# Optimization experiments

Hardware: AMD Instinct MI355X
Metric: run time of the kernel (lower is better)

The kernel has to match this reference:

```python
import jax, jax.numpy as jnp
import numpy as np
from jax import lax

B = 1024
T = 32           # length_sec = 384 // (2*2*3*1)
HGT = 7          # height_image = 28 // (1*2*2*1)
CC = 32          # last conv channels
AD = HGT * CC    # abstract_dim = 224
HID = 256        # attention decoder hidden
VOCAB = 29
OUT_LEN = 25


def setup_inputs() -> dict:
    ks = jax.random.split(jax.random.key(0), 24)
    n = lambda k, s, sc=1.0: jax.random.normal(k, s, jnp.float32) * sc
    return {
        "x": n(ks[0], (B, 1, 384, 28)),
        "conv1_w": n(ks[1], (4, 1, 3, 3), 0.2),   "conv1_b": n(ks[2], (4,), 0.1),
        "conv2_w": n(ks[3], (16, 4, 3, 3), 0.2),  "conv2_b": n(ks[4], (16,), 0.1),
        "conv3_w": n(ks[5], (16, 16, 3, 3), 0.2), "conv3_b": n(ks[6], (16,), 0.1),
        "conv4_w": n(ks[7], (32, 16, 3, 3), 0.2), "conv4_b": n(ks[8], (32,), 0.1),
        "h0": n(ks[9], (1, AD)), "c0": n(ks[10], (1, AD)),
        "lstm_Wih": n(ks[11], (4 * AD, AD), 0.05), "lstm_Whh": n(ks[12], (4 * AD, AD), 0.05),
        "lstm_bih": n(ks[13], (4 * AD,), 0.05),    "lstm_bhh": n(ks[14], (4 * AD,), 0.05),
        "att_w": n(ks[15], (1, HID + AD), 0.05),   "att_b": n(ks[16], (1,), 0.05),
        "dec_Wih": n(ks[17], (4 * HID, AD), 0.05), "dec_Whh": n(ks[18], (4 * HID, HID), 0.05),
        "dec_bih": n(ks[19], (4 * HID,), 0.05),    "dec_bhh": n(ks[20], (4 * HID,), 0.05),
        "out_w": n(ks[21], (VOCAB, HID), 0.05),    "out_b": n(ks[22], (VOCAB,), 0.05),
    }


def _lstm_cell(h, c, xt, Wih, Whh, bih, bhh):
    # PyTorch gate order: i, f, g, o
    g = xt @ Wih.T + bih + h @ Whh.T + bhh
    i, f, gg, o = jnp.split(g, 4, axis=-1)
    c = jax.nn.sigmoid(f) * c + jax.nn.sigmoid(i) * jnp.tanh(gg)
    h = jax.nn.sigmoid(o) * jnp.tanh(c)
    return h, c


def reference(x, conv1_w, conv1_b, conv2_w, conv2_b, conv3_w, conv3_b, conv4_w, conv4_b,
              h0, c0, lstm_Wih, lstm_Whh, lstm_bih, lstm_bhh,
              att_w, att_b, dec_Wih, dec_Whh, dec_bih, dec_bhh, out_w, out_b):
    def crp(z, w, b, pool):
        y = lax.conv_general_dilated(z, w, (1, 1), [(1, 1), (1, 1)],
                                     dimension_numbers=('NCHW', 'OIHW', 'NCHW'))
        y = jax.nn.relu(y + b[None, :, None, None])
        win = (1, 1) + pool
        return lax.reduce_window(y, -jnp.inf, lax.max, win, win, 'VALID')

    y1 = crp(x, conv1_w, conv1_b, (2, 1))
    y2 = crp(y1, conv2_w, conv2_b, (2, 2))
    y3 = crp(y2, conv3_w, conv3_b, (3, 2))
    y4 = crp(y3, conv4_w, conv4_b, (1, 1))          # [B, 32, 32, 7]
    Bsz = x.shape[0]
    # y5[b,t,i] = y4[b, i%32, t, i//32]  ==  transpose + reshape (replaces python loop)
    y5 = jnp.transpose(y4, (0, 2, 3, 1)).reshape(Bsz, T, AD)   # [B, T, 224]

    # encoder LSTM (seq-major scan, like torch LSTM)
    def estep(carry, xt):
        h, c = carry
        h, c = _lstm_cell(h, c, xt, lstm_Wih, lstm_Whh, lstm_bih, lstm_bhh)
        return (h, c), h
    h0b = jnp.tile(h0, (Bsz, 1))
    c0b = jnp.tile(c0, (Bsz, 1))
    _, hs = lax.scan(estep, (h0b, c0b), jnp.transpose(y5, (1, 0, 2)))
    y8 = jnp.transpose(hs, (1, 0, 2))                # [B, T, 224]

    # attention decoder: additive score softmax(linear(concat(h, enc)))
    w_h = att_w[0, :HID]     # hidden part
    w_e = att_w[0, HID:]     # encoder part
    enc_score = y8 @ w_e     # [B, T], precomputed once

    def dstep(carry, _):
        h, c = carry
        scores = enc_score + (h @ w_h)[:, None] + att_b[0]      # [B, T]
        alpha = jax.nn.softmax(scores, axis=1)
        ctx = jnp.einsum('bt,btd->bd', alpha, y8)               # [B, 224]
        h, c = _lstm_cell(h, c, ctx, dec_Wih, dec_Whh, dec_bih, dec_bhh)
        return (h, c), h @ out_w.T + out_b                      # [B, 29]

    hdec = jnp.zeros((Bsz, HID), x.dtype)
    _, outs = lax.scan(dstep, (hdec, hdec), None, length=OUT_LEN)  # [25, B, 29]
    return jnp.transpose(outs, (1, 2, 0))            # [B, 29, 25]
```

## Files before the change

kernel.cpp:

```cpp
#include <hip/hip_runtime.h>

typedef unsigned short u16;
typedef unsigned int u32;
typedef unsigned long long u64;
typedef __bf16 bfrag __attribute__((ext_vector_type(8)));
typedef float v4f __attribute__((ext_vector_type(4)));

#define DI __device__ __forceinline__

DI float bf2f(u16 b){ union{u32 u; float f;} c; c.u = ((u32)b)<<16; return c.f; }
DI u16 f2bf(float f){ union{float f; u32 u;} c; c.f=f; u32 u=c.u; return (u16)((u + 0x7FFFu + ((u>>16)&1u))>>16); }
DI float sigm(float x){ return 1.0f/(1.0f+__expf(-x)); }
DI float tanhf_(float x){ float a=fabsf(x); float e=__expf(2.0f*a); float r=1.0f-2.0f/(e+1.0f); return x<0.0f? -r : r; }

__global__ __launch_bounds__(256) void k_cvt2(const float* __restrict__ src, u16* __restrict__ hi,
                                              u16* __restrict__ lo, u32 n){
  u32 i = blockIdx.x*256u + threadIdx.x;
  if (i < n){ float v = src[i]; u16 h = f2bf(v); hi[i] = h; lo[i] = f2bf(v - bf2f(h)); }
}

__global__ __launch_bounds__(256) void k_conv1(const float* __restrict__ x, const float* __restrict__ w,
                                               const float* __restrict__ bias, float* __restrict__ y1q, u32 bbase){
  u32 gid = blockIdx.x*256u + threadIdx.x;
  u32 bl = gid/768u, r = gid - bl*768u;
  u32 oy = r>>2, xg = r&3u;
  const float* xb = x + (u64)(bbase+bl)*10752u;
  float win[4][9];
  #pragma unroll
  for (int rr=0; rr<4; rr++){
    int iy = 2*(int)oy - 1 + rr;
    bool vy = (u32)iy < 384u;
    #pragma unroll
    for (int cc=0; cc<9; cc++){
      int ix = (int)(xg*7u) + cc - 1;
      win[rr][cc] = (vy && (u32)ix < 28u) ? xb[iy*28 + ix] : 0.0f;
    }
  }
  #pragma unroll
  for (int co=0; co<4; co++){
    float wf[9];
    #pragma unroll
    for (int j=0;j<9;j++) wf[j] = w[co*9+j];
    float bc = bias[co];
    float* outp = y1q + ((u64)(bl*4u+co)*192u + oy)*28u + xg*7u;
    #pragma unroll
    for (int ox=0; ox<7; ox++){
      float m = 0.0f;
      #pragma unroll
      for (int py=0; py<2; py++){
        float s = bc;
        #pragma unroll
        for (int dy=0; dy<3; dy++)
          #pragma unroll
          for (int dx=0; dx<3; dx++)
            s += win[py+dy][ox+dx]*wf[dy*3+dx];
        m = fmaxf(m, s);
      }
      outp[ox] = m;
    }
  }
}

__global__ __launch_bounds__(256) void k_conv2(const float* __restrict__ y1q, const float* __restrict__ w,
                                               const float* __restrict__ bias, float* __restrict__ y2q){
  u32 gid = blockIdx.x*256u + threadIdx.x;
  u32 bl = gid/1536u, r = gid - bl*1536u;
  u32 oy = r>>4, xg = (r>>3)&1u, cp = r&7u;
  const float* inb = y1q + (u64)bl*21504u;
  float acc[2][7][4];
  #pragma unroll
  for (int c2=0;c2<2;c2++)
    #pragma unroll
    for (int i=0;i<7;i++){ acc[c2][i][0]=0.f;acc[c2][i][1]=0.f;acc[c2][i][2]=0.f;acc[c2][i][3]=0.f; }
  for (int ci=0; ci<4; ci++){
    float win[4][16];
    const float* pl = inb + ci*5376;
    #pragma unroll
    for (int rr=0; rr<4; rr++){
      int iy = 2*(int)oy - 1 + rr;
      bool vy = (u32)iy < 192u;
      #pragma unroll
      for (int cc=0; cc<16; cc++){
        int ix = (int)(xg*14u) + cc - 1;
        win[rr][cc] = (vy && (u32)ix<28u) ? pl[iy*28+ix] : 0.0f;
      }
    }
    float wf[2][9];
    #pragma unroll
    for (int c2=0;c2<2;c2++)
      #pragma unroll
      for (int j=0;j<9;j++) wf[c2][j] = w[((cp*2u+(u32)c2)*4u+(u32)ci)*9u+j];
    #pragma unroll
    for (int c2=0;c2<2;c2++)
      #pragma unroll
      for (int ol=0; ol<7; ol++)
        #pragma unroll
        for (int py=0; py<2; py++)
          #pragma unroll
          for (int px=0; px<2; px++){
            float s = acc[c2][ol][py*2+px];
            #pragma unroll
            for (int dy=0; dy<3; dy++)
              #pragma unroll
              for (int dx=0; dx<3; dx++)
                s += win[py+dy][2*ol+px+dx]*wf[c2][dy*3+dx];
            acc[c2][ol][py*2+px] = s;
          }
  }
  #pragma unroll
  for (int c2=0;c2<2;c2++){
    u32 co = cp*2u+(u32)c2;
    float bc = bias[co];
    float* outp = y2q + ((u64)(bl*16u+co)*96u + oy)*14u + xg*7u;
    #pragma unroll
    for (int ol=0; ol<7; ol++){
      float m = fmaxf(fmaxf(acc[c2][ol][0],acc[c2][ol][1]), fmaxf(acc[c2][ol][2],acc[c2][ol][3])) + bc;
      outp[ol] = fmaxf(m, 0.0f);
    }
  }
}

__global__ __launch_bounds__(256) void k_conv3(const float* __restrict__ y2q, const float* __restrict__ w,
                                               const float* __restrict__ bias, float* __restrict__ y3, u32 bbase){
  u32 gid = blockIdx.x*256u + threadIdx.x;
  u32 bl = gid/512u, r = gid - bl*512u;
  u32 oy = r>>4, co = r&15u;
  const float* inb = y2q + (u64)bl*21504u;
  float acc[7][6];
  #pragma unroll
  for (int i=0;i<7;i++){
    #pragma unroll
    for (int j=0;j<6;j++) acc[i][j]=0.0f;
  }
  for (int ci=0; ci<16; ci++){
    float win[5][16];
    const float* pl = inb + ci*1344;
    #pragma unroll
    for (int rr=0; rr<5; rr++){
      int iy = 3*(int)oy - 1 + rr;
      bool vy = (u32)iy < 96u;
      #pragma unroll
      for (int cc=0; cc<16; cc++){
        int ix = cc-1;
        win[rr][cc] = (vy && (u32)ix<14u) ? pl[iy*14+ix] : 0.0f;
      }
    }
    float wf[9];
    #pragma unroll
    for (int j=0;j<9;j++) wf[j] = w[((u32)co*16u+(u32)ci)*9u+j];
    #pragma unroll
    for (int ox=0; ox<7; ox++){
      #pragma unroll
      for (int py=0; py<3; py++)
        #pragma unroll
        for (int px=0; px<2; px++){
          float s = acc[ox][py*2+px];
          #pragma unroll
          for (int dy=0; dy<3; dy++)
            #pragma unroll
            for (int dx=0; dx<3; dx++)
              s += win[py+dy][2*ox+px+dx]*wf[dy*3+dx];
          acc[ox][py*2+px] = s;
        }
    }
  }
  float bc = bias[co];
  float* outp = y3 + ((u64)((bbase+bl)*16u+co)*32u + oy)*7u;
  #pragma unroll
  for (int ox=0; ox<7; ox++){
    float m = acc[ox][0];
    #pragma unroll
    for (int j=1;j<6;j++) m = fmaxf(m, acc[ox][j]);
    outp[ox] = fmaxf(m + bc, 0.0f);
  }
}

__global__ __launch_bounds__(256) void k_conv4(const float* __restrict__ y3, const float* __restrict__ w,
                                               const float* __restrict__ bias, float* __restrict__ y5){
  u32 gid = blockIdx.x*256u + threadIdx.x;
  u32 b = gid/512u, r = gid - b*512u;
  u32 oy = r>>4, cp = r&15u;
  u32 co0 = cp*2u;
  const float* inb = y3 + (u64)b*3584u;
  float acc[2][7];
  #pragma unroll
  for (int i=0;i<2;i++){
    #pragma unroll
    for (int j=0;j<7;j++) acc[i][j]=0.0f;
  }
  for (int ci=0; ci<16; ci++){
    float win[3][9];
    const float* pl = inb + ci*224;
    #pragma unroll
    for (int rr=0; rr<3; rr++){
      int iy = (int)oy - 1 + rr;
      bool vy = (u32)iy < 32u;
      #pragma unroll
      for (int cc=0; cc<9; cc++){
        int ix = cc-1;
        win[rr][cc] = (vy && (u32)ix<7u) ? pl[iy*7+ix] : 0.0f;
      }
    }
    #pragma unroll
    for (int c2=0; c2<2; c2++){
      float wf[9];
      #pragma unroll
      for (int j=0;j<9;j++) wf[j] = w[((co0+(u32)c2)*16u+(u32)ci)*9u+j];
      #pragma unroll
      for (int ox=0; ox<7; ox++){
        float s = acc[c2][ox];
        #pragma unroll
        for (int dy=0; dy<3; dy++)
          #pragma unroll
          for (int dx=0; dx<3; dx++)
            s += win[dy][ox+dx]*wf[dy*3+dx];
        acc[c2][ox] = s;
      }
    }
  }
  #pragma unroll
  for (int c2=0; c2<2; c2++){
    float bc = bias[co0+(u32)c2];
    #pragma unroll
    for (int ox=0; ox<7; ox++)
      y5[((u64)b*32u + oy)*224u + (u32)ox*32u + (co0+(u32)c2)] = fmaxf(acc[c2][ox] + bc, 0.0f);
  }
}

__global__ __launch_bounds__(1024) void k_zero(u32* __restrict__ p){
  p[threadIdx.x] = 0u;
}

__global__ __launch_bounds__(512, 4) void k_enc7(const u16* __restrict__ WihHi, const u16* __restrict__ WihLo,
                                                 const u16* __restrict__ WhhHi, const u16* __restrict__ WhhLo,
                                                 const float* __restrict__ bih, const float* __restrict__ bhh,
                                                 const float* __restrict__ y5, const float* __restrict__ h0,
                                                 const float* __restrict__ c0, float* __restrict__ y8,
                                                 u32* __restrict__ eflags){
  __shared__ __align__(16) u16 Ahi[16*456], Alo[16*456];
  __shared__ __align__(16) float gsh[16*132];
  __shared__ __align__(16) float bsh[128];
  u32 tid = threadIdx.x, w = tid>>6, lane = tid&63u, nl = lane&15u, quad = lane>>4;
  u32 bid = blockIdx.x, g = bid & 63u, q = bid >> 6;
  u32 b0 = g*16u, hc0 = q*32u;
  if (tid < 128u){
    u32 gi = tid>>5, col = gi*224u + hc0 + (tid&31u);
    bsh[tid] = bih[col] + bhh[col];
  }
  for (u32 it=tid; it<3584u; it+=512u){
    u32 r = it/224u, c = it - r*224u;
    float v = h0[c]; u16 hb = f2bf(v);
    Ahi[r*456u+224u+c] = hb; Alo[r*456u+224u+c] = f2bf(v - bf2f(hb));
  }
  float creg = c0[hc0 + (tid&31u)];
  u32* fE = eflags + g*16u;
  const u32 col = (w>>1)*224u + hc0 + (w&1u)*16u + nl;
  const u32 gl  = (w>>1)*32u  + (w&1u)*16u + nl;
  __syncthreads();
  for (u32 t=0; t<32u; t++){
    #pragma unroll
    for (int i=0;i<7;i++){
      u32 item = (u32)i*512u + tid;
      u32 r = item/224u, c = item - r*224u;
      float v = y5[((u64)(b0+r)*32u + t)*224u + c];
      u16 hb = f2bf(v);
      Ahi[r*456u+c] = hb; Alo[r*456u+c] = f2bf(v - bf2f(hb));
    }
    __syncthreads();
    v4f acc = {};
    #pragma unroll
    for (int kt=0; kt<14; kt++){
      u32 ka = (u32)kt*32u + quad*8u;
      bfrag ah = *(const bfrag*)&Ahi[nl*456u + ka];
      bfrag al = *(const bfrag*)&Alo[nl*456u + ka];
      bfrag bh, bl;
      if (kt<7){
        u64 o = (u64)col*224u + ka;
        bh = *(const bfrag*)&WihHi[o]; bl = *(const bfrag*)&WihLo[o];
      } else {
        u64 o = (u64)col*224u + (ka - 224u);
        bh = *(const bfrag*)&WhhHi[o]; bl = *(const bfrag*)&WhhLo[o];
      }
      acc = __builtin_amdgcn_mfma_f32_16x16x32_bf16(ah, bh, acc, 0,0,0);
      acc = __builtin_amdgcn_mfma_f32_16x16x32_bf16(al, bh, acc, 0,0,0);
      acc = __builtin_amdgcn_mfma_f32_16x16x32_bf16(ah, bl, acc, 0,0,0);
    }
    #pragma unroll
    for (int rg=0; rg<4; rg++)
      gsh[(quad*4u+(u32)rg)*132u + gl] = acc[rg];
    __syncthreads();
    {
      u32 row = tid>>5, hl = tid&31u;
      float gi_ = gsh[row*132u +       hl] + bsh[hl];
      float gf_ = gsh[row*132u + 32u + hl] + bsh[32u+hl];
      float gg_ = gsh[row*132u + 64u + hl] + bsh[64u+hl];
      float go_ = gsh[row*132u + 96u + hl] + bsh[96u+hl];
      float cv = sigm(gf_)*creg + sigm(gi_)*tanhf_(gg_);
      float hv = sigm(go_)*tanhf_(cv);
      creg = cv;
      union{float f; u32 u;} cu; cu.f = hv;
      __hip_atomic_store((u32*)&y8[((u64)(b0+row)*32u + t)*224u + hc0 + hl], cu.u,
                         __ATOMIC_RELAXED, __HIP_MEMORY_SCOPE_AGENT);
    }
    __syncthreads();
    if (tid==0u)
      __hip_atomic_fetch_add(fE, 1u, __ATOMIC_RELEASE, __HIP_MEMORY_SCOPE_AGENT);
    if (t < 31u){
      if (tid==0u){
        while (__hip_atomic_load(fE, __ATOMIC_RELAXED, __HIP_MEMORY_SCOPE_AGENT) < 7u*(t+1u))
          __builtin_amdgcn_s_sleep(2);
      }
      __syncthreads();
      for (u32 it=tid; it<3584u; it+=512u){
        u32 r = it/224u, c = it - r*224u;
        u32 uv = __hip_atomic_load((const u32*)&y8[((u64)(b0+r)*32u + t)*224u + c],
                                   __ATOMIC_RELAXED, __HIP_MEMORY_SCOPE_AGENT);
        union{u32 u; float f;} cu; cu.u = uv;
        u16 hb = f2bf(cu.f);
        Ahi[r*456u+224u+c] = hb; Alo[r*456u+224u+c] = f2bf(cu.f - bf2f(hb));
      }
    }
  }
}

__global__ __launch_bounds__(512) void k_dec4(const float* __restrict__ y8,
    const float* __restrict__ attw, const float* __restrict__ attb,
    const u16* __restrict__ WihHi, const u16* __restrict__ WihLo,
    const u16* __restrict__ WhhHi, const u16* __restrict__ WhhLo,
    const float* __restrict__ bih, const float* __restrict__ bhh,
    u32* __restrict__ hist, u32* __restrict__ ctxc, u32* __restrict__ flags){
  __shared__ __align__(16) u16 Ahi[16*488], Alo[16*488];
  __shared__ __align__(16) float hfull[16*256];
  __shared__ __align__(16) float gsh[16*260];
  __shared__ __align__(16) float esc[16*33];
  __shared__ __align__(16) float alp[16*33];
  __shared__ __align__(16) float bsh[256];
  u32 tid=threadIdx.x, w=tid>>6, lane=tid&63u, nl=lane&15u, quad=lane>>4;
  u32 p = blockIdx.x, xcd = p&7u, slot = p>>3;
  u32 q = xcd>>1;
  u32 g = (xcd&1u)*32u + slot;
  u32 b0 = g*16u, hc0 = q*64u;
  for (u32 it=tid; it<256u; it+=512u){
    u32 gi = it>>6, col = gi*256u + hc0 + (it&63u);
    bsh[it] = bih[col] + bhh[col];
  }
  for (u32 it=tid; it<4096u; it+=512u){
    u32 r=it>>8, c=it&255u;
    Ahi[r*488u+224u+c]=0; Alo[r*488u+224u+c]=0;
    hfull[it]=0.0f;
  }
  {
    u32 r=tid>>5, t=tid&31u;
    const float* yr = y8 + ((u64)(b0+r)*32u + t)*224u;
    const float* we = attw + 256;
    float sacc=0.0f;
    #pragma unroll 8
    for (int j=0;j<224;j++) sacc += yr[j]*we[j];
    esc[r*33u+t] = sacc + attb[0];
  }
  float cst[2] = {0.0f, 0.0f};
  u32* fh = flags + g*16u;
  u32* fc = flags + g*16u + 8u;
  const u32 nt0 = w, nt1 = w + 8u;
  const u32 col0 = (nt0>>2)*256u + hc0 + (nt0&3u)*16u + nl;
  const u32 col1 = (nt1>>2)*256u + hc0 + (nt1&3u)*16u + nl;
  const u32 gl0  = (nt0>>2)*64u + (nt0&3u)*16u + nl;
  const u32 gl1  = (nt1>>2)*64u + (nt1&3u)*16u + nl;
  __syncthreads();
  for (u32 s=0; s<25u; s++){
    if (s>0u){
      if (tid==0u){
        while (__hip_atomic_load(fh, __ATOMIC_RELAXED, __HIP_MEMORY_SCOPE_AGENT) < 4u*s)
          __builtin_amdgcn_s_sleep(2);
      }
      __syncthreads();
      u32* hrow = hist + ((u64)(s-1u)*1024u + b0)*256u;
      for (u32 it=tid; it<4096u; it+=512u){
        u32 v = __hip_atomic_load(&hrow[it], __ATOMIC_RELAXED, __HIP_MEMORY_SCOPE_AGENT);
        u32 r = it>>8, c = it&255u;
        u16 hb = (u16)(v>>16), lb = (u16)(v&0xFFFFu);
        Ahi[r*488u+224u+c] = hb; Alo[r*488u+224u+c] = lb;
        hfull[it] = bf2f(hb) + bf2f(lb);
      }
      __syncthreads();
    }
    {
      u32 r=tid>>5, t=tid&31u;
      float part=0.0f;
      if (s>0u){
        #pragma unroll
        for (int qq=0; qq<8; qq++){
          u32 c = t + (u32)qq*32u;
          part += hfull[r*256u+c]*attw[c];
        }
        #pragma unroll
        for (int off=16; off; off>>=1) part += __shfl_xor(part, off, 32);
      }
      float sv = esc[r*33u+t] + part;
      float mx = sv;
      #pragma unroll
      for (int off=16; off; off>>=1) mx = fmaxf(mx, __shfl_xor(mx, off, 32));
      float e = __expf(sv-mx);
      float ssum = e;
      #pragma unroll
      for (int off=16; off; off>>=1) ssum += __shfl_xor(ssum, off, 32);
      alp[r*33u+t] = e/ssum;
    }
    __syncthreads();
    u32* cdst = ctxc + (u64)(s&1u)*229376u + (u64)g*3584u;
    for (u32 it=tid; it<896u; it+=512u){
      u32 rr = it/56u, cc = it - rr*56u + q*56u;
      const float* yb = y8 + (u64)(b0+rr)*32u*224u + cc;
      float a0=0.0f;
      #pragma unroll
      for (int tt=0; tt<32; tt++) a0 += alp[rr*33u+(u32)tt]*yb[(u32)tt*224u];
      u16 hb = f2bf(a0), lb = f2bf(a0 - bf2f(hb));
      __hip_atomic_store(&cdst[rr*224u+cc], ((u32)hb<<16)|(u32)lb, __ATOMIC_RELAXED, __HIP_MEMORY_SCOPE_AGENT);
    }
    __syncthreads();
    if (tid==0u)
      __hip_atomic_fetch_add(fc, 1u, __ATOMIC_RELEASE, __HIP_MEMORY_SCOPE_AGENT);
    v4f acc0 = {}, acc1 = {};
    #pragma unroll
    for (int kt=7; kt<15; kt++){
      u32 ka = (u32)kt*32u + quad*8u;
      bfrag afh = *(const bfrag*)&Ahi[nl*488u + ka];
      bfrag afl = *(const bfrag*)&Alo[nl*488u + ka];
      u32 kb = ka - 224u;
      u64 o0 = (u64)col0*256u + kb, o1 = (u64)col1*256u + kb;
      bfrag b0h = *(const bfrag*)&WhhHi[o0], b0l = *(const bfrag*)&WhhLo[o0];
      bfrag b1h = *(const bfrag*)&WhhHi[o1], b1l = *(const bfrag*)&WhhLo[o1];
      acc0 = __builtin_amdgcn_mfma_f32_16x16x32_bf16(afh, b0h, acc0, 0,0,0);
      acc0 = __builtin_amdgcn_mfma_f32_16x16x32_bf16(afl, b0h, acc0, 0,0,0);
      acc0 = __builtin_amdgcn_mfma_f32_16x16x32_bf16(afh, b0l, acc0, 0,0,0);
      acc1 = __builtin_amdgcn_mfma_f32_16x16x32_bf16(afh, b1h, acc1, 0,0,0);
      acc1 = __builtin_amdgcn_mfma_f32_16x16x32_bf16(afl, b1h, acc1, 0,0,0);
      acc1 = __builtin_amdgcn_mfma_f32_16x16x32_bf16(afh, b1l, acc1, 0,0,0);
    }
    if (tid==0u){
      while (__hip_atomic_load(fc, __ATOMIC_RELAXED, __HIP_MEMORY_SCOPE_AGENT) < 4u*(s+1u))
        __builtin_amdgcn_s_sleep(2);
    }
    __syncthreads();
    for (u32 it=tid; it<3584u; it+=512u){
      u32 v = __hip_atomic_load(&cdst[it], __ATOMIC_RELAXED, __HIP_MEMORY_SCOPE_AGENT);
      u32 rr = it/224u, cc = it - rr*224u;
      Ahi[rr*488u+cc] = (u16)(v>>16); Alo[rr*488u+cc] = (u16)(v&0xFFFFu);
    }
    __syncthreads();
    #pragma unroll
    for (int kt=0; kt<7; kt++){
      u32 ka = (u32)kt*32u + quad*8u;
      bfrag afh = *(const bfrag*)&Ahi[nl*488u + ka];
      bfrag afl = *(const bfrag*)&Alo[nl*488u + ka];
      u64 o0 = (u64)col0*224u + ka, o1 = (u64)col1*224u + ka;
      bfrag b0h = *(const bfrag*)&WihHi[o0], b0l = *(const bfrag*)&WihLo[o0];
      bfrag b1h = *(const bfrag*)&WihHi[o1], b1l = *(const bfrag*)&WihLo[o1];
      acc0 = __builtin_amdgcn_mfma_f32_16x16x32_bf16(afh, b0h, acc0, 0,0,0);
      acc0 = __builtin_amdgcn_mfma_f32_16x16x32_bf16(afl, b0h, acc0, 0,0,0);
      acc0 = __builtin_amdgcn_mfma_f32_16x16x32_bf16(afh, b0l, acc0, 0,0,0);
      acc1 = __builtin_amdgcn_mfma_f32_16x16x32_bf16(afh, b1h, acc1, 0,0,0);
      acc1 = __builtin_amdgcn_mfma_f32_16x16x32_bf16(afl, b1h, acc1, 0,0,0);
      acc1 = __builtin_amdgcn_mfma_f32_16x16x32_bf16(afh, b1l, acc1, 0,0,0);
    }
    #pragma unroll
    for (int rg=0; rg<4; rg++){
      gsh[(quad*4u+(u32)rg)*260u + gl0] = acc0[rg];
      gsh[(quad*4u+(u32)rg)*260u + gl1] = acc1[rg];
    }
    __syncthreads();
    u32* hdst = hist + ((u64)s*1024u + b0)*256u + hc0;
    #pragma unroll
    for (int k2=0; k2<2; k2++){
      u32 l = (u32)k2*512u + tid;
      u32 row = l>>6, hl = l&63u;
      float gi_ = gsh[row*260u + hl]         + bsh[hl];
      float gf_ = gsh[row*260u + 64u  + hl]  + bsh[64u+hl];
      float gg_ = gsh[row*260u + 128u + hl]  + bsh[128u+hl];
      float go_ = gsh[row*260u + 192u + hl]  + bsh[192u+hl];
      float cv = sigm(gf_)*cst[k2] + sigm(gi_)*tanhf_(gg_);
      float hv = sigm(go_)*tanhf_(cv);
      cst[k2] = cv;
      u16 hb = f2bf(hv), lb = f2bf(hv - bf2f(hb));
      __hip_atomic_store(&hdst[row*256u + hl], ((u32)hb<<16)|(u32)lb, __ATOMIC_RELAXED, __HIP_MEMORY_SCOPE_AGENT);
    }
    __syncthreads();
    if (tid==0u)
      __hip_atomic_fetch_add(fh, 1u, __ATOMIC_RELEASE, __HIP_MEMORY_SCOPE_AGENT);
  }
}

__global__ __launch_bounds__(256) void k_out(const u32* __restrict__ hist, const float* __restrict__ outw,
                                             const float* __restrict__ outb, float* __restrict__ outp){
  __shared__ __align__(16) float wsh[29*260];
  __shared__ __align__(16) float hrow[256];
  u32 tid = threadIdx.x, b = blockIdx.x;
  for (u32 it=tid; it<7424u; it+=256u){
    u32 v = it/256u, c = it&255u;
    wsh[v*260u+c] = outw[v*256u+c];
  }
  __syncthreads();
  for (u32 s=0; s<25u; s++){
    u32 v = hist[((u64)s*1024u + b)*256u + tid];
    hrow[tid] = bf2f((u16)(v>>16)) + bf2f((u16)(v&0xFFFFu));
    __syncthreads();
    if (tid < 232u){
      u32 vv = tid>>3, k8 = tid&7u;
      float a = 0.0f;
      #pragma unroll
      for (int j=0;j<32;j++) a += hrow[k8*32u+(u32)j]*wsh[vv*260u + k8*32u + (u32)j];
      #pragma unroll
      for (int off=4; off; off>>=1) a += __shfl_xor(a, off, 8);
      if (k8==0u) outp[((u64)b*29u + vv)*25u + s] = a + outb[vv];
    }
    __syncthreads();
  }
}

extern "C" void kernel_launch(void* const* d_in, const int* in_sizes, int n_in,
                              void* d_out, int out_size, void* d_ws, size_t ws_size,
                              hipStream_t stream){
  (void)in_sizes; (void)n_in; (void)out_size; (void)ws_size;
  const float* x    = (const float*)d_in[0];
  const float* c1w  = (const float*)d_in[1];
  const float* c1b  = (const float*)d_in[2];
  const float* c2w  = (const float*)d_in[3];
  const float* c2b  = (const float*)d_in[4];
  const float* c3w  = (const float*)d_in[5];
  const float* c3b  = (const float*)d_in[6];
  const float* c4w  = (const float*)d_in[7];
  const float* c4b  = (const float*)d_in[8];
  const float* h0   = (const float*)d_in[9];
  const float* c0   = (const float*)d_in[10];
  const float* lWih = (const float*)d_in[11];
  const float* lWhh = (const float*)d_in[12];
  const float* lbih = (const float*)d_in[13];
  const float* lbhh = (const float*)d_in[14];
  const float* attw = (const float*)d_in[15];
  const float* attb = (const float*)d_in[16];
  const float* dWih = (const float*)d_in[17];
  const float* dWhh = (const float*)d_in[18];
  const float* dbih = (const float*)d_in[19];
  const float* dbhh = (const float*)d_in[20];
  const float* outw = (const float*)d_in[21];
  const float* outb = (const float*)d_in[22];
  float* out = (float*)d_out;
  char* ws = (char*)d_ws;
  float* y1q = (float*)(ws);
  float* y2q = (float*)(ws + 22020096ull);
  float* y3  = (float*)(ws + 44040192ull);
  float* y5  = (float*)(ws);
  float* y8  = (float*)(ws + 29360128ull);
  u32* hist  = (u32*)(ws);
  u32* ctxc  = (u32*)(ws + 26214400ull);
  u32* flags = (u32*)(ws + 28049408ull);
  u16* lWihHi = (u16*)(ws + 58720256ull);
  u16* lWihLo = (u16*)(ws + 59121664ull);
  u16* lWhhHi = (u16*)(ws + 59523072ull);
  u16* lWhhLo = (u16*)(ws + 59924480ull);
  u16* dWihHi = (u16*)(ws + 60325888ull);
  u16* dWihLo = (u16*)(ws + 60784640ull);
  u16* dWhhHi = (u16*)(ws + 61243392ull);
  u16* dWhhLo = (u16*)(ws + 61767680ull);
  u32* eflags = (u32*)d_out;

  k_cvt2<<<dim3(784),  dim3(256), 0, stream>>>(lWih, lWihHi, lWihLo, 200704u);
  k_cvt2<<<dim3(784),  dim3(256), 0, stream>>>(lWhh, lWhhHi, lWhhLo, 200704u);
  k_cvt2<<<dim3(896),  dim3(256), 0, stream>>>(dWih, dWihHi, dWihLo, 229376u);
  k_cvt2<<<dim3(1024), dim3(256), 0, stream>>>(dWhh, dWhhHi, dWhhLo, 262144u);
  for (u32 q=0; q<4; q++){
    k_conv1<<<dim3(768),  dim3(256), 0, stream>>>(x, c1w, c1b, y1q, q*256u);
    k_conv2<<<dim3(1536), dim3(256), 0, stream>>>(y1q, c2w, c2b, y2q);
    k_conv3<<<dim3(512),  dim3(256), 0, stream>>>(y2q, c3w, c3b, y3, q*256u);
  }
  k_conv4<<<dim3(2048), dim3(256), 0, stream>>>(y3, c4w, c4b, y5);
  k_zero <<<dim3(1), dim3(1024), 0, stream>>>(eflags);
  k_enc7 <<<dim3(448), dim3(512), 0, stream>>>(lWihHi, lWihLo, lWhhHi, lWhhLo, lbih, lbhh,
                                               y5, h0, c0, y8, eflags);
  k_zero <<<dim3(1), dim3(1024), 0, stream>>>(flags);
  k_dec4 <<<dim3(256), dim3(512), 0, stream>>>(y8, attw, attb, dWihHi, dWihLo, dWhhHi, dWhhLo,
                                               dbih, dbhh, hist, ctxc, flags);
  k_out  <<<dim3(1024), dim3(256), 0, stream>>>(hist, outw, outb, out);
}
```

Baseline: 2.075 ms.

## Split decoder LSTM across eight blocks per batch group instead of four

The persistent attention decoder now gives each 16-row batch group eight cooperating blocks, each owning 32 hidden columns, instead of four blocks of 64 columns. That doubles the grid to 512 blocks and halves the MFMA and weight-load work per block per step. Shared memory per block also shrinks: hfull and esc are dropped, with the attention partial rebuilt from the hi/lo bf16 copies and the encoder score kept in a register. The flag thresholds scale to eight blocks, and launch bounds ask for four blocks per CU. The risk is more cross-block spin-wait traffic, and co-residency of all 512 blocks is needed to avoid deadlock.

```diff
diff --git a/kernel.cpp b/kernel.cpp
--- a/kernel.cpp
+++ b/kernel.cpp
@@ -323,32 +323,28 @@
   }
 }
 
-__global__ __launch_bounds__(512) void k_dec4(const float* __restrict__ y8,
+__global__ __launch_bounds__(512, 4) void k_dec8(const float* __restrict__ y8,
     const float* __restrict__ attw, const float* __restrict__ attb,
     const u16* __restrict__ WihHi, const u16* __restrict__ WihLo,
     const u16* __restrict__ WhhHi, const u16* __restrict__ WhhLo,
     const float* __restrict__ bih, const float* __restrict__ bhh,
     u32* __restrict__ hist, u32* __restrict__ ctxc, u32* __restrict__ flags){
   __shared__ __align__(16) u16 Ahi[16*488], Alo[16*488];
-  __shared__ __align__(16) float hfull[16*256];
-  __shared__ __align__(16) float gsh[16*260];
-  __shared__ __align__(16) float esc[16*33];
+  __shared__ __align__(16) float gsh[16*132];
   __shared__ __align__(16) float alp[16*33];
-  __shared__ __align__(16) float bsh[256];
+  __shared__ __align__(16) float bsh[128];
   u32 tid=threadIdx.x, w=tid>>6, lane=tid&63u, nl=lane&15u, quad=lane>>4;
-  u32 p = blockIdx.x, xcd = p&7u, slot = p>>3;
-  u32 q = xcd>>1;
-  u32 g = (xcd&1u)*32u + slot;
-  u32 b0 = g*16u, hc0 = q*64u;
-  for (u32 it=tid; it<256u; it+=512u){
-    u32 gi = it>>6, col = gi*256u + hc0 + (it&63u);
-    bsh[it] = bih[col] + bhh[col];
+  u32 bid = blockIdx.x, g = bid>>3, q = bid&7u;
+  u32 b0 = g*16u, hc0 = q*32u;
+  if (tid < 128u){
+    u32 gi = tid>>5, col = gi*256u + hc0 + (tid&31u);
+    bsh[tid] = bih[col] + bhh[col];
   }
   for (u32 it=tid; it<4096u; it+=512u){
     u32 r=it>>8, c=it&255u;
     Ahi[r*488u+224u+c]=0; Alo[r*488u+224u+c]=0;
-    hfull[it]=0.0f;
-  }
+  }
+  float escr;
   {
     u32 r=tid>>5, t=tid&31u;
     const float* yr = y8 + ((u64)(b0+r)*32u + t)*224u;
@@ -356,21 +352,19 @@
     float sacc=0.0f;
     #pragma unroll 8
     for (int j=0;j<224;j++) sacc += yr[j]*we[j];
-    esc[r*33u+t] = sacc + attb[0];
-  }
-  float cst[2] = {0.0f, 0.0f};
+    escr = sacc + attb[0];
+  }
+  float cst = 0.0f;
   u32* fh = flags + g*16u;
   u32* fc = flags + g*16u + 8u;
-  const u32 nt0 = w, nt1 = w + 8u;
-  const u32 col0 = (nt0>>2)*256u + hc0 + (nt0&3u)*16u + nl;
-  const u32 col1 = (nt1>>2)*256u + hc0 + (nt1&3u)*16u + nl;
-  const u32 gl0  = (nt0>>2)*64u + (nt0&3u)*16u + nl;
-  const u32 gl1  = (nt1>>2)*64u + (nt1&3u)*16u + nl;
+  const u32 colG = (w>>1)*256u + hc0 + (w&1u)*16u + nl;
+  const u32 gl   = (w>>1)*32u  + (w&1u)*16u + nl;
+  const u32 rrE = tid/28u, ccE = (tid - rrE*28u) + q*28u;
   __syncthreads();
   for (u32 s=0; s<25u; s++){
     if (s>0u){
       if (tid==0u){
-        while (__hip_atomic_load(fh, __ATOMIC_RELAXED, __HIP_MEMORY_SCOPE_AGENT) < 4u*s)
+        while (__hip_atomic_load(fh, __ATOMIC_RELAXED, __HIP_MEMORY_SCOPE_AGENT) < 8u*s)
           __builtin_amdgcn_s_sleep(2);
       }
       __syncthreads();
@@ -378,9 +372,7 @@
       for (u32 it=tid; it<4096u; it+=512u){
         u32 v = __hip_atomic_load(&hrow[it], __ATOMIC_RELAXED, __HIP_MEMORY_SCOPE_AGENT);
         u32 r = it>>8, c = it&255u;
-        u16 hb = (u16)(v>>16), lb = (u16)(v&0xFFFFu);
-        Ahi[r*488u+224u+c] = hb; Alo[r*488u+224u+c] = lb;
-        hfull[it] = bf2f(hb) + bf2f(lb);
+        Ahi[r*488u+224u+c] = (u16)(v>>16); Alo[r*488u+224u+c] = (u16)(v&0xFFFFu);
       }
       __syncthreads();
     }
@@ -391,12 +383,13 @@
         #pragma unroll
         for (int qq=0; qq<8; qq++){
           u32 c = t + (u32)qq*32u;
-          part += hfull[r*256u+c]*attw[c];
+          float hvf = bf2f(Ahi[r*488u+224u+c]) + bf2f(Alo[r*488u+224u+c]);
+          part += hvf*attw[c];
         }
         #pragma unroll
         for (int off=16; off; off>>=1) part += __shfl_xor(part, off, 32);
       }
-      float sv = esc[r*33u+t] + part;
+      float sv = escr + part;
       float mx = sv;
       #pragma unroll
       for (int off=16; off; off>>=1) mx = fmaxf(mx, __shfl_xor(mx, off, 32));
@@ -408,37 +401,32 @@
     }
     __syncthreads();
     u32* cdst = ctxc + (u64)(s&1u)*229376u + (u64)g*3584u;
-    for (u32 it=tid; it<896u; it+=512u){
-      u32 rr = it/56u, cc = it - rr*56u + q*56u;
-      const float* yb = y8 + (u64)(b0+rr)*32u*224u + cc;
+    if (tid < 448u){
+      const float* yb = y8 + (u64)(b0+rrE)*7168u + ccE;
       float a0=0.0f;
       #pragma unroll
-      for (int tt=0; tt<32; tt++) a0 += alp[rr*33u+(u32)tt]*yb[(u32)tt*224u];
+      for (int tt=0; tt<32; tt++) a0 += alp[rrE*33u+(u32)tt]*yb[(u32)tt*224u];
       u16 hb = f2bf(a0), lb = f2bf(a0 - bf2f(hb));
-      __hip_atomic_store(&cdst[rr*224u+cc], ((u32)hb<<16)|(u32)lb, __ATOMIC_RELAXED, __HIP_MEMORY_SCOPE_AGENT);
+      __hip_atomic_store(&cdst[rrE*224u+ccE], ((u32)hb<<16)|(u32)lb, __ATOMIC_RELAXED, __HIP_MEMORY_SCOPE_AGENT);
     }
     __syncthreads();
     if (tid==0u)
       __hip_atomic_fetch_add(fc, 1u, __ATOMIC_RELEASE, __HIP_MEMORY_SCOPE_AGENT);
-    v4f acc0 = {}, acc1 = {};
+    v4f acc = {};
     #pragma unroll
     for (int kt=7; kt<15; kt++){
       u32 ka = (u32)kt*32u + quad*8u;
       bfrag afh = *(const bfrag*)&Ahi[nl*488u + ka];
       bfrag afl = *(const bfrag*)&Alo[nl*488u + ka];
       u32 kb = ka - 224u;
-      u64 o0 = (u64)col0*256u + kb, o1 = (u64)col1*256u + kb;
-      bfrag b0h = *(const bfrag*)&WhhHi[o0], b0l = *(const bfrag*)&WhhLo[o0];
-      bfrag b1h = *(const bfrag*)&WhhHi[o1], b1l = *(const bfrag*)&WhhLo[o1];
-      acc0 = __builtin_amdgcn_mfma_f32_16x16x32_bf16(afh, b0h, acc0, 0,0,0);
-      acc0 = __builtin_amdgcn_mfma_f32_16x16x32_bf16(afl, b0h, acc0, 0,0,0);
-      acc0 = __builtin_amdgcn_mfma_f32_16x16x32_bf16(afh, b0l, acc0, 0,0,0);
-      acc1 = __builtin_amdgcn_mfma_f32_16x16x32_bf16(afh, b1h, acc1, 0,0,0);
-      acc1 = __builtin_amdgcn_mfma_f32_16x16x32_bf16(afl, b1h, acc1, 0,0,0);
-      acc1 = __builtin_amdgcn_mfma_f32_16x16x32_bf16(afh, b1l, acc1, 0,0,0);
+      u64 o = (u64)colG*256u + kb;
+      bfrag bh = *(const bfrag*)&WhhHi[o], bl = *(const bfrag*)&WhhLo[o];
+      acc = __builtin_amdgcn_mfma_f32_16x16x32_bf16(afh, bh, acc, 0,0,0);
+      acc = __builtin_amdgcn_mfma_f32_16x16x32_bf16(afl, bh, acc, 0,0,0);
+      acc = __builtin_amdgcn_mfma_f32_16x16x32_bf16(afh, bl, acc, 0,0,0);
     }
     if (tid==0u){
-      while (__hip_atomic_load(fc, __ATOMIC_RELAXED, __HIP_MEMORY_SCOPE_AGENT) < 4u*(s+1u))
+      while (__hip_atomic_load(fc, __ATOMIC_RELAXED, __HIP_MEMORY_SCOPE_AGENT) < 8u*(s+1u))
         __builtin_amdgcn_s_sleep(2);
     }
     __syncthreads();
@@ -453,36 +441,28 @@
       u32 ka = (u32)kt*32u + quad*8u;
       bfrag afh = *(const bfrag*)&Ahi[nl*488u + ka];
       bfrag afl = *(const bfrag*)&Alo[nl*488u + ka];
-      u64 o0 = (u64)col0*224u + ka, o1 = (u64)col1*224u + ka;
-      bfrag b0h = *(const bfrag*)&WihHi[o0], b0l = *(const bfrag*)&WihLo[o0];
-      bfrag b1h = *(const bfrag*)&WihHi[o1], b1l = *(const bfrag*)&WihLo[o1];
-      acc0 = __builtin_amdgcn_mfma_f32_16x16x32_bf16(afh, b0h, acc0, 0,0,0);
-      acc0 = __builtin_amdgcn_mfma_f32_16x16x32_bf16(afl, b0h, acc0, 0,0,0);
-      acc0 = __builtin_amdgcn_mfma_f32_16x16x32_bf16(afh, b0l, acc0, 0,0,0);
-      acc1 = __builtin_amdgcn_mfma_f32_16x16x32_bf16(afh, b1h, acc1, 0,0,0);
-      acc1 = __builtin_amdgcn_mfma_f32_16x16x32_bf16(afl, b1h, acc1, 0,0,0);
-      acc1 = __builtin_amdgcn_mfma_f32_16x16x32_bf16(afh, b1l, acc1, 0,0,0);
-    }
-    #pragma unroll
-    for (int rg=0; rg<4; rg++){
-      gsh[(quad*4u+(u32)rg)*260u + gl0] = acc0[rg];
-      gsh[(quad*4u+(u32)rg)*260u + gl1] = acc1[rg];
-    }
-    __syncthreads();
-    u32* hdst = hist + ((u64)s*1024u + b0)*256u + hc0;
-    #pragma unroll
-    for (int k2=0; k2<2; k2++){
-      u32 l = (u32)k2*512u + tid;
-      u32 row = l>>6, hl = l&63u;
-      float gi_ = gsh[row*260u + hl]         + bsh[hl];
-      float gf_ = gsh[row*260u + 64u  + hl]  + bsh[64u+hl];
-      float gg_ = gsh[row*260u + 128u + hl]  + bsh[128u+hl];
-      float go_ = gsh[row*260u + 192u + hl]  + bsh[192u+hl];
-      float cv = sigm(gf_)*cst[k2] + sigm(gi_)*tanhf_(gg_);
+      u64 o = (u64)colG*224u + ka;
+      bfrag bh = *(const bfrag*)&WihHi[o], bl = *(const bfrag*)&WihLo[o];
+      acc = __builtin_amdgcn_mfma_f32_16x16x32_bf16(afh, bh, acc, 0,0,0);
+      acc = __builtin_amdgcn_mfma_f32_16x16x32_bf16(afl, bh, acc, 0,0,0);
+      acc = __builtin_amdgcn_mfma_f32_16x16x32_bf16(afh, bl, acc, 0,0,0);
+    }
+    #pragma unroll
+    for (int rg=0; rg<4; rg++)
+      gsh[(quad*4u+(u32)rg)*132u + gl] = acc[rg];
+    __syncthreads();
+    {
+      u32 row = tid>>5, hl = tid&31u;
+      float gi_ = gsh[row*132u +       hl] + bsh[hl];
+      float gf_ = gsh[row*132u + 32u + hl] + bsh[32u+hl];
+      float gg_ = gsh[row*132u + 64u + hl] + bsh[64u+hl];
+      float go_ = gsh[row*132u + 96u + hl] + bsh[96u+hl];
+      float cv = sigm(gf_)*cst + sigm(gi_)*tanhf_(gg_);
       float hv = sigm(go_)*tanhf_(cv);
-      cst[k2] = cv;
+      cst = cv;
       u16 hb = f2bf(hv), lb = f2bf(hv - bf2f(hb));
-      __hip_atomic_store(&hdst[row*256u + hl], ((u32)hb<<16)|(u32)lb, __ATOMIC_RELAXED, __HIP_MEMORY_SCOPE_AGENT);
+      __hip_atomic_store(&hist[((u64)s*1024u + b0 + row)*256u + hc0 + hl],
+                         ((u32)hb<<16)|(u32)lb, __ATOMIC_RELAXED, __HIP_MEMORY_SCOPE_AGENT);
     }
     __syncthreads();
     if (tid==0u)
@@ -578,7 +558,7 @@
   k_enc7 <<<dim3(448), dim3(512), 0, stream>>>(lWihHi, lWihLo, lWhhHi, lWhhLo, lbih, lbhh,
                                                y5, h0, c0, y8, eflags);
   k_zero <<<dim3(1), dim3(1024), 0, stream>>>(flags);
-  k_dec4 <<<dim3(256), dim3(512), 0, stream>>>(y8, attw, attb, dWihHi, dWihLo, dWhhHi, dWhhLo,
+  k_dec8 <<<dim3(512), dim3(512), 0, stream>>>(y8, attw, attb, dWihHi, dWihLo, dWhhHi, dWhhLo,
                                                dbih, dbhh, hist, ctxc, flags);
   k_out  <<<dim3(1024), dim3(256), 0, stream>>>(hist, outw, outb, out);
 }
```

After: 2.662 ms. 1.28x slower.
